# Kernel tuning notes

Measured on AMD Instinct MI355X. Metric: run time of the kernel, lower is better.

The kernel has to match this reference:

```python
import jax, jax.numpy as jnp
import numpy as np

D_MODEL = 1024
N_HEADS = 16
D_FF = 4096
EPS = 1e-5


def setup_inputs() -> dict:
    key = jax.random.key(0)
    ks = jax.random.split(key, 10)
    B, S, D, F = 4, 2048, D_MODEL, D_FF
    s = 0.02
    return {
        "x": jax.random.normal(ks[0], (B, S, D), jnp.float32),
        "Wq": jax.random.normal(ks[1], (D, D), jnp.float32) * s,
        "bq": jnp.zeros((D,), jnp.float32),
        "Wk": jax.random.normal(ks[2], (D, D), jnp.float32) * s,
        "bk": jnp.zeros((D,), jnp.float32),
        "Wv": jax.random.normal(ks[3], (D, D), jnp.float32) * s,
        "bv": jnp.zeros((D,), jnp.float32),
        "Wo": jax.random.normal(ks[4], (D, D), jnp.float32) * s,
        "bo": jnp.zeros((D,), jnp.float32),
        "ln1_g": jnp.ones((D,), jnp.float32),
        "ln1_b": jnp.zeros((D,), jnp.float32),
        "ln2_g": jnp.ones((D,), jnp.float32),
        "ln2_b": jnp.zeros((D,), jnp.float32),
        "W1": jax.random.normal(ks[5], (D, F), jnp.float32) * s,
        "b1": jnp.zeros((F,), jnp.float32),
        "W2": jax.random.normal(ks[6], (F, D), jnp.float32) * s,
        "b2": jnp.zeros((D,), jnp.float32),
    }


def _layernorm(x, g, b):
    mu = jnp.mean(x, axis=-1, keepdims=True)
    var = jnp.mean(jnp.square(x - mu), axis=-1, keepdims=True)
    return (x - mu) * jax.lax.rsqrt(var + EPS) * g + b


def _attention(x, Wq, bq, Wk, bk, Wv, bv, Wo, bo):
    B, S, D = x.shape
    H, dk = N_HEADS, D // N_HEADS
    q = (x @ Wq + bq).reshape(B, S, H, dk).transpose(0, 2, 1, 3)  # bhsd
    k = (x @ Wk + bk).reshape(B, S, H, dk).transpose(0, 2, 1, 3)
    v = (x @ Wv + bv).reshape(B, S, H, dk).transpose(0, 2, 1, 3)
    scale = 1.0 / np.sqrt(dk)
    scores = jnp.einsum("bhqd,bhkd->bhqk", q, k) * scale
    causal = jnp.tril(jnp.ones((S, S), bool))
    scores = jnp.where(causal, scores, -jnp.inf)
    attn = jax.nn.softmax(scores, axis=-1)
    out = jnp.einsum("bhqk,bhkd->bhqd", attn, v)
    out = out.transpose(0, 2, 1, 3).reshape(B, S, D)
    return out @ Wo + bo


def reference(x, Wq, bq, Wk, bk, Wv, bv, Wo, bo, ln1_g, ln1_b, ln2_g, ln2_b, W1, b1, W2, b2):
    # Pre-LN: x -> LN -> attn -> +x -> LN -> FFN -> +x  (dropout = eval/identity)
    attn_out = _attention(_layernorm(x, ln1_g, ln1_b), Wq, bq, Wk, bk, Wv, bv, Wo, bo)
    x = x + attn_out
    h = _layernorm(x, ln2_g, ln2_b)
    ffn = jax.nn.gelu(h @ W1 + b1, approximate=False) @ W2 + b2
    return x + ffn
```

## Files before the change

### kernel.cpp

```cpp
#include <hip/hip_runtime.h>
#include <hip/hip_bf16.h>
#include <math.h>

typedef __attribute__((ext_vector_type(8))) short short8;
typedef __attribute__((ext_vector_type(4))) float floatx4;
typedef __attribute__((ext_vector_type(4))) short short4v;
typedef __attribute__((ext_vector_type(2))) unsigned int uint2v;

#define D_MODEL 1024
#define N_HEADS 16
#define DK 64
#define D_FF 4096
#define BB 4
#define SS 2048
#define NTOK (BB * SS)
#define LN_EPS 1e-5f
#define SCL 0.18033688011112042f

static __device__ __forceinline__ short f2bf(float f) {
  union { float f; unsigned int u; } v;
  v.f = f;
  unsigned int u = v.u;
  unsigned int r = u + 0x7fffu + ((u >> 16) & 1u);
  return (short)(r >> 16);
}

#define GLL16(g, l)                                                            \
  __builtin_amdgcn_global_load_lds(                                            \
      (const __attribute__((address_space(1))) void*)(g),                      \
      (__attribute__((address_space(3))) void*)(l), 16, 0, 0)

__global__ __launch_bounds__(256) void ln_kernel(const float* __restrict__ x,
                                                 const float* __restrict__ g,
                                                 const float* __restrict__ b,
                                                 short* __restrict__ out) {
  int row = blockIdx.x;
  int t = threadIdx.x;
  const float4* rp = (const float4*)(x + (size_t)row * D_MODEL);
  float4 v = rp[t];
  float s = v.x + v.y + v.z + v.w;
  float ss = v.x * v.x + v.y * v.y + v.z * v.z + v.w * v.w;
#pragma unroll
  for (int off = 32; off >= 1; off >>= 1) {
    s += __shfl_xor(s, off, 64);
    ss += __shfl_xor(ss, off, 64);
  }
  __shared__ float red[8];
  int wv = t >> 6;
  if ((t & 63) == 0) { red[wv] = s; red[wv + 4] = ss; }
  __syncthreads();
  s = red[0] + red[1] + red[2] + red[3];
  ss = red[4] + red[5] + red[6] + red[7];
  float mu = s * (1.0f / D_MODEL);
  float var = ss * (1.0f / D_MODEL) - mu * mu;
  float rstd = rsqrtf(var + LN_EPS);
  float4 gv = ((const float4*)g)[t];
  float4 bv = ((const float4*)b)[t];
  short4v o;
  o.x = f2bf((v.x - mu) * rstd * gv.x + bv.x);
  o.y = f2bf((v.y - mu) * rstd * gv.y + bv.y);
  o.z = f2bf((v.z - mu) * rstd * gv.z + bv.z);
  o.w = f2bf((v.w - mu) * rstd * gv.w + bv.w);
  *(short4v*)(out + (size_t)row * D_MODEL + t * 4) = o;
}

__global__ __launch_bounds__(256) void wconvert_all(
    const float* __restrict__ Wq, const float* __restrict__ Wk,
    const float* __restrict__ Wv, const float* __restrict__ Wo,
    const float* __restrict__ W1, const float* __restrict__ W2,
    const float* __restrict__ bq, const float* __restrict__ bk,
    const float* __restrict__ bv,
    short* __restrict__ wqkv_t, short* __restrict__ wo_t,
    short* __restrict__ w1_t, short* __restrict__ w2_t,
    float* __restrict__ bqkv) {
  __shared__ float tile[64][65];
  int id = blockIdx.x;
  int t = threadIdx.x;
  if (id == 3072) {
    for (int i = t; i < 1024; i += 256) {
      bqkv[i] = bq[i] * SCL;
      bqkv[1024 + i] = bk[i];
      bqkv[2048 + i] = bv[i];
    }
    return;
  }
  const float* W;
  short* Wt;
  int K, N, tid;
  float scale = 1.0f;
  if (id < 1024) {
    int wsel = id >> 8;
    tid = id & 255;
    K = 1024; N = 1024;
    W = wsel == 0 ? Wq : wsel == 1 ? Wk : wsel == 2 ? Wv : Wo;
    Wt = wsel < 3 ? wqkv_t + (size_t)wsel * 1024 * 1024 : wo_t;
    if (wsel == 0) scale = SCL;
  } else if (id < 2048) {
    tid = id - 1024; K = 1024; N = 4096; W = W1; Wt = w1_t;
  } else {
    tid = id - 2048; K = 4096; N = 1024; W = W2; Wt = w2_t;
  }
  int ntn = N >> 6;
  int n0 = (tid % ntn) * 64, k0 = (tid / ntn) * 64;
  int c = t & 63, r0 = t >> 6;
#pragma unroll
  for (int i = 0; i < 16; i++) {
    int r = r0 + i * 4;
    tile[r][c] = W[(size_t)(k0 + r) * N + n0 + c];
  }
  __syncthreads();
#pragma unroll
  for (int i = 0; i < 16; i++) {
    int r = r0 + i * 4;
    Wt[(size_t)(n0 + r) * K + k0 + c] = f2bf(tile[c][r] * scale);
  }
}

template <int MODE>
__global__ __launch_bounds__(256, 4) void gemm_bt(const short* __restrict__ A,
                                                  const short* __restrict__ Bt,
                                                  const float* __restrict__ bias,
                                                  const float* __restrict__ res,
                                                  float* __restrict__ outf,
                                                  short* __restrict__ outb,
                                                  int M, int N, int K) {
  __shared__ short As[128 * 64];
  __shared__ short Bs[128 * 64];
  int t = threadIdx.x;
  int w = t >> 6, l = t & 63;
  int lm = l & 15, lq = l >> 4;
  int nx = gridDim.x;
  int id = blockIdx.y * nx + blockIdx.x;
  int xcd = id & 7;
  int k = id >> 3;
  int rows_per = gridDim.y >> 3;
  int mt = xcd * rows_per + k / nx;
  int nt = k - (k / nx) * nx;
  int m0 = mt * 128, n0 = nt * 128;
  floatx4 acc[4][4] = {};
  int l3 = l >> 3;
  int c7 = ((l & 7) ^ l3) * 8;
  const short* aA = A + (size_t)(m0 + w * 8 + l3) * K + c7;
  const short* aB = Bt + (size_t)(n0 + w * 8 + l3) * K + c7;
  int wm = (w & 1) * 64, wn = (w >> 1) * 64;
  int sw = lm & 7;

  for (int kt = 0; kt < K; kt += 64) {
#pragma unroll
    for (int j = 0; j < 4; j++) {
      GLL16(aA + (size_t)(j * 32) * K, As + (j * 32 + w * 8) * 64);
      GLL16(aB + (size_t)(j * 32) * K, Bs + (j * 32 + w * 8) * 64);
    }
    aA += 64;
    aB += 64;
    __syncthreads();
#pragma unroll
    for (int kk = 0; kk < 2; kk++) {
      int rdoff = ((kk * 4 + lq) ^ sw) * 8;
      short8 af[4], bfr[4];
#pragma unroll
      for (int mi = 0; mi < 4; mi++)
        af[mi] = *(const short8*)&As[(wm + mi * 16 + lm) * 64 + rdoff];
#pragma unroll
      for (int ni = 0; ni < 4; ni++)
        bfr[ni] = *(const short8*)&Bs[(wn + ni * 16 + lm) * 64 + rdoff];
#pragma unroll
      for (int mi = 0; mi < 4; mi++)
#pragma unroll
        for (int ni = 0; ni < 4; ni++)
          acc[mi][ni] = __builtin_amdgcn_mfma_f32_16x16x32_bf16(af[mi], bfr[ni],
                                                                acc[mi][ni], 0, 0, 0);
    }
    __syncthreads();
  }

#pragma unroll
  for (int mi = 0; mi < 4; mi++) {
#pragma unroll
    for (int ni = 0; ni < 4; ni++) {
      int col = n0 + wn + ni * 16 + lm;
      float bcol = bias[col];
#pragma unroll
      for (int r = 0; r < 4; r++) {
        int row = m0 + wm + mi * 16 + lq * 4 + r;
        float v = acc[mi][ni][r] + bcol;
        size_t idx = (size_t)row * N + col;
        if (MODE == 0) {
          outb[idx] = f2bf(v);
        } else if (MODE == 1) {
          outf[idx] = v + res[idx];
        } else {
          float vc = v + 0.044715f * v * v * v;
          float e = __builtin_amdgcn_exp2f(2.302265246314f * vc);
          float ge = v * e * __builtin_amdgcn_rcpf(e + 1.0f);
          outb[idx] = f2bf(ge);
        }
      }
    }
  }
}

__global__ __launch_bounds__(256) void vtrans(const short* __restrict__ qkv,
                                              short* __restrict__ vt) {
  __shared__ short Ls[64][72];
  int t = threadIdx.x;
  int s0 = blockIdx.x * 64;
  int bh = blockIdx.y;
  int b = bh >> 4, h = bh & 15;
  const short* vsrc = qkv + (size_t)b * SS * 3072 + 2048 + h * 64;
#pragma unroll
  for (int it = 0; it < 2; it++) {
    int idx = it * 256 + t;
    int sr = idx >> 3, ch = idx & 7;
    *(short8*)&Ls[sr][ch * 8] =
        *(const short8*)&vsrc[(size_t)(s0 + sr) * 3072 + ch * 8];
  }
  __syncthreads();
  int d = t >> 2, sb = (t & 3) * 16;
  short tmp[16];
#pragma unroll
  for (int j = 0; j < 16; j++) tmp[j] = Ls[sb + j][d];
  short8* dst = (short8*)&vt[(size_t)bh * DK * SS + (size_t)d * SS + s0 + sb];
  dst[0] = *(short8*)&tmp[0];
  dst[1] = *(short8*)&tmp[8];
}

__global__ __launch_bounds__(256, 3) void attn_kernel(const short* __restrict__ qkv,
                                                      const short* __restrict__ vt,
                                                      short* __restrict__ o) {
  __shared__ short Qs[128 * 64];
  __shared__ short Ks[64 * 64];
  __shared__ short Vs[80 * 64];
  __shared__ short Ps[128 * 72];
  int t = threadIdx.x, w = t >> 6, l = t & 63;
  int bh = blockIdx.x;
  int qi = 15 - blockIdx.y;
  int b = bh >> 4, h = bh & 15;
  const short* qbase = qkv + (size_t)b * SS * 3072 + h * DK;
  const short* kbase = qbase + 1024;
  const short* vbase = vt + (size_t)bh * DK * SS;
  short* obase = o + (size_t)b * SS * D_MODEL + h * DK;
  int l7 = l & 7, l3 = l >> 3;
  int c7 = (l7 ^ l3) * 8;
  int lm = l & 15, lq = l >> 4;
  int swq = lm & 7;
  int q0 = qi * 128;

  {
    int r = 64 + (t >> 4);
    int c = (t & 15) * 4;
    short val = (r == 64) ? (short)0x3F80 : (short)0;
    short4v vv = {val, val, val, val};
    *(short4v*)&Vs[r * 64 + c] = vv;
  }
#pragma unroll
  for (int j = 0; j < 4; j++) {
    int r8 = w * 32 + j * 8;
    GLL16(qbase + (size_t)(q0 + r8 + l3) * 3072 + c7, Qs + r8 * 64);
  }
  __syncthreads();
  short8 aq[2][2];
#pragma unroll
  for (int m = 0; m < 2; m++)
#pragma unroll
    for (int hf = 0; hf < 2; hf++)
      aq[m][hf] = *(const short8*)&Qs[(w * 32 + m * 16 + lm) * 64 +
                                      ((hf * 4 + lq) ^ swq) * 8];

  floatx4 accO[2][4] = {};
  floatx4 accL[2] = {};
  int qrow[2] = {q0 + w * 32 + lm, q0 + w * 32 + 16 + lm};
  int wrow_min = q0 + w * 32;
  int wrow_max = wrow_min + 31;
  int ntile = 2 * qi + 2;
  for (int kt = 0; kt < ntile; kt++) {
    int k0 = kt * 64;
    __syncthreads();
#pragma unroll
    for (int j = 0; j < 2; j++) {
      int r8 = (w * 2 + j) * 8;
      GLL16(kbase + (size_t)(k0 + r8 + l3) * 3072 + c7, Ks + r8 * 64);
      GLL16(vbase + (size_t)(r8 + l3) * SS + k0 + c7, Vs + r8 * 64);
    }
    __syncthreads();

    if (k0 <= wrow_max) {
      floatx4 sc[4][2];
#pragma unroll
      for (int sb = 0; sb < 4; sb++) {
        short8 k0f = *(const short8*)&Ks[(sb * 16 + lm) * 64 + (lq ^ swq) * 8];
        short8 k1f =
            *(const short8*)&Ks[(sb * 16 + lm) * 64 + ((4 + lq) ^ swq) * 8];
#pragma unroll
        for (int m = 0; m < 2; m++) {
          floatx4 z = {};
          z = __builtin_amdgcn_mfma_f32_16x16x32_bf16(k0f, aq[m][0], z, 0, 0, 0);
          z = __builtin_amdgcn_mfma_f32_16x16x32_bf16(k1f, aq[m][1], z, 0, 0, 0);
          sc[sb][m] = z;
        }
      }
      if (k0 + 63 <= wrow_min) {
#pragma unroll
        for (int sb = 0; sb < 4; sb++)
#pragma unroll
          for (int m = 0; m < 2; m++)
#pragma unroll
            for (int r = 0; r < 4; r++)
              sc[sb][m][r] = __builtin_amdgcn_exp2f(sc[sb][m][r]);
      } else {
#pragma unroll
        for (int sb = 0; sb < 4; sb++) {
          int sbase = k0 + sb * 16 + lq * 4;
#pragma unroll
          for (int m = 0; m < 2; m++)
#pragma unroll
            for (int r = 0; r < 4; r++)
              sc[sb][m][r] = (sbase + r > qrow[m])
                                 ? 0.f
                                 : __builtin_amdgcn_exp2f(sc[sb][m][r]);
        }
      }
#pragma unroll
      for (int m = 0; m < 2; m++)
#pragma unroll
        for (int sb = 0; sb < 4; sb++) {
          union { float f; unsigned int u; } c0, c1, c2, c3;
          c0.f = sc[sb][m][0]; c1.f = sc[sb][m][1];
          c2.f = sc[sb][m][2]; c3.f = sc[sb][m][3];
          uint2v pk;
          pk.x = __builtin_amdgcn_perm(c1.u, c0.u, 0x07060302u);
          pk.y = __builtin_amdgcn_perm(c3.u, c2.u, 0x07060302u);
          *(uint2v*)&Ps[(w * 32 + m * 16 + lm) * 72 + sb * 16 + lq * 4] = pk;
        }
      short8 pa[2][2];
#pragma unroll
      for (int m = 0; m < 2; m++)
#pragma unroll
        for (int hf = 0; hf < 2; hf++)
          pa[m][hf] =
              *(const short8*)&Ps[(w * 32 + m * 16 + lm) * 72 + hf * 32 + lq * 8];
      short8 o0 = *(const short8*)&Vs[(64 + lm) * 64 + (lq ^ swq) * 8];
      short8 o1 = *(const short8*)&Vs[(64 + lm) * 64 + ((4 + lq) ^ swq) * 8];
#pragma unroll
      for (int m = 0; m < 2; m++) {
        accL[m] = __builtin_amdgcn_mfma_f32_16x16x32_bf16(pa[m][0], o0, accL[m], 0, 0, 0);
        accL[m] = __builtin_amdgcn_mfma_f32_16x16x32_bf16(pa[m][1], o1, accL[m], 0, 0, 0);
      }
#pragma unroll
      for (int nb = 0; nb < 4; nb++) {
        short8 v0f = *(const short8*)&Vs[(nb * 16 + lm) * 64 + (lq ^ swq) * 8];
        short8 v1f =
            *(const short8*)&Vs[(nb * 16 + lm) * 64 + ((4 + lq) ^ swq) * 8];
#pragma unroll
        for (int m = 0; m < 2; m++) {
          accO[m][nb] = __builtin_amdgcn_mfma_f32_16x16x32_bf16(pa[m][0], v0f,
                                                                accO[m][nb], 0, 0, 0);
          accO[m][nb] = __builtin_amdgcn_mfma_f32_16x16x32_bf16(pa[m][1], v1f,
                                                                accO[m][nb], 0, 0, 0);
        }
      }
    }
  }
#pragma unroll
  for (int m = 0; m < 2; m++) {
#pragma unroll
    for (int r = 0; r < 4; r++) {
      float lv = __shfl(accL[m][r], l & 48, 64);
      float invr = __builtin_amdgcn_rcpf(lv);
      int rowg = q0 + w * 32 + m * 16 + lq * 4 + r;
#pragma unroll
      for (int nb = 0; nb < 4; nb++)
        obase[(size_t)rowg * D_MODEL + nb * 16 + lm] = f2bf(accO[m][nb][r] * invr);
    }
  }
}

extern "C" void kernel_launch(void* const* d_in, const int* in_sizes, int n_in,
                              void* d_out, int out_size, void* d_ws, size_t ws_size,
                              hipStream_t stream) {
  const float* x = (const float*)d_in[0];
  const float* Wq = (const float*)d_in[1];
  const float* bq = (const float*)d_in[2];
  const float* Wk = (const float*)d_in[3];
  const float* bk = (const float*)d_in[4];
  const float* Wv = (const float*)d_in[5];
  const float* bv = (const float*)d_in[6];
  const float* Wo = (const float*)d_in[7];
  const float* bo = (const float*)d_in[8];
  const float* ln1g = (const float*)d_in[9];
  const float* ln1b = (const float*)d_in[10];
  const float* ln2g = (const float*)d_in[11];
  const float* ln2b = (const float*)d_in[12];
  const float* W1 = (const float*)d_in[13];
  const float* b1 = (const float*)d_in[14];
  const float* W2 = (const float*)d_in[15];
  const float* b2 = (const float*)d_in[16];
  float* out = (float*)d_out;

  short* wqkv_t = (short*)d_ws;
  short* wo_t = wqkv_t + 3072 * 1024;
  short* w1_t = wo_t + 1024 * 1024;
  short* w2_t = w1_t + 4096 * 1024;
  float* bqkv = (float*)(w2_t + 1024 * 4096);
  short* h_bf = (short*)(bqkv + 3072);
  short* qkvb = h_bf + (size_t)NTOK * D_MODEL;
  short* vtg = qkvb + (size_t)NTOK * 3072;
  short* ffn1 = qkvb;

  wconvert_all<<<3073, 256, 0, stream>>>(Wq, Wk, Wv, Wo, W1, W2, bq, bk, bv,
                                         wqkv_t, wo_t, w1_t, w2_t, bqkv);

  ln_kernel<<<NTOK, 256, 0, stream>>>(x, ln1g, ln1b, h_bf);

  gemm_bt<0><<<dim3(24, 64), 256, 0, stream>>>(h_bf, wqkv_t, bqkv, nullptr, nullptr,
                                               qkvb, NTOK, 3072, 1024);

  vtrans<<<dim3(SS / 64, 64), 256, 0, stream>>>(qkvb, vtg);

  attn_kernel<<<dim3(64, 16), 256, 0, stream>>>(qkvb, vtg, h_bf);

  gemm_bt<1><<<dim3(8, 64), 256, 0, stream>>>(h_bf, wo_t, bo, x, out, nullptr,
                                              NTOK, 1024, 1024);

  ln_kernel<<<NTOK, 256, 0, stream>>>(out, ln2g, ln2b, h_bf);

  gemm_bt<2><<<dim3(32, 64), 256, 0, stream>>>(h_bf, w1_t, b1, nullptr, nullptr,
                                               ffn1, NTOK, 4096, 1024);

  gemm_bt<1><<<dim3(8, 64), 256, 0, stream>>>(ffn1, w2_t, b2, out, out, nullptr,
                                              NTOK, 1024, 4096);
}
```

Measured before the change: 465.8 us.

## Fuse all stages into one persistent cooperative kernel with grid syncs

```diff
diff --git a/kernel.cpp b/kernel.cpp
--- a/kernel.cpp
+++ b/kernel.cpp
@@ -1,6 +1,9 @@
 #include <hip/hip_runtime.h>
 #include <hip/hip_bf16.h>
+#include <hip/hip_cooperative_groups.h>
 #include <math.h>
+
+namespace cg = cooperative_groups;
 
 typedef __attribute__((ext_vector_type(8))) short short8;
 typedef __attribute__((ext_vector_type(4))) float floatx4;
@@ -16,6 +19,7 @@
 #define NTOK (BB * SS)
 #define LN_EPS 1e-5f
 #define SCL 0.18033688011112042f
+#define NBLK 768
 
 static __device__ __forceinline__ short f2bf(float f) {
   union { float f; unsigned int u; } v;
@@ -30,11 +34,11 @@
       (const __attribute__((address_space(1))) void*)(g),                      \
       (__attribute__((address_space(3))) void*)(l), 16, 0, 0)
 
-__global__ __launch_bounds__(256) void ln_kernel(const float* __restrict__ x,
-                                                 const float* __restrict__ g,
-                                                 const float* __restrict__ b,
-                                                 short* __restrict__ out) {
-  int row = blockIdx.x;
+
+__device__ __forceinline__ void dev_ln_row(int row, const float* x,
+                                           const float* g, const float* b,
+                                           short* out, char* smem) {
+  float* red = (float*)smem;
   int t = threadIdx.x;
   const float4* rp = (const float4*)(x + (size_t)row * D_MODEL);
   float4 v = rp[t];
@@ -45,7 +49,6 @@
     s += __shfl_xor(s, off, 64);
     ss += __shfl_xor(ss, off, 64);
   }
-  __shared__ float red[8];
   int wv = t >> 6;
   if ((t & 63) == 0) { red[wv] = s; red[wv + 4] = ss; }
   __syncthreads();
@@ -64,17 +67,11 @@
   *(short4v*)(out + (size_t)row * D_MODEL + t * 4) = o;
 }
 
-__global__ __launch_bounds__(256) void wconvert_all(
-    const float* __restrict__ Wq, const float* __restrict__ Wk,
-    const float* __restrict__ Wv, const float* __restrict__ Wo,
-    const float* __restrict__ W1, const float* __restrict__ W2,
-    const float* __restrict__ bq, const float* __restrict__ bk,
-    const float* __restrict__ bv,
-    short* __restrict__ wqkv_t, short* __restrict__ wo_t,
-    short* __restrict__ w1_t, short* __restrict__ w2_t,
-    float* __restrict__ bqkv) {
-  __shared__ float tile[64][65];
-  int id = blockIdx.x;
+__device__ __forceinline__ void dev_wconv(
+    int id, const float* Wq, const float* Wk, const float* Wv, const float* Wo,
+    const float* W1, const float* W2, const float* bq, const float* bk,
+    const float* bv, short* wqkv_t, short* wo_t, short* w1_t, short* w2_t,
+    float* bqkv, char* smem) {
   int t = threadIdx.x;
   if (id == 3072) {
     for (int i = t; i < 1024; i += 256) {
@@ -84,6 +81,7 @@
     }
     return;
   }
+  float (*tile)[65] = (float (*)[65])smem;
   const float* W;
   short* Wt;
   int K, N, tid;
@@ -117,26 +115,14 @@
 }
 
 template <int MODE>
-__global__ __launch_bounds__(256, 4) void gemm_bt(const short* __restrict__ A,
-                                                  const short* __restrict__ Bt,
-                                                  const float* __restrict__ bias,
-                                                  const float* __restrict__ res,
-                                                  float* __restrict__ outf,
-                                                  short* __restrict__ outb,
-                                                  int M, int N, int K) {
-  __shared__ short As[128 * 64];
-  __shared__ short Bs[128 * 64];
+__device__ __forceinline__ void dev_gemm_tile(
+    const short* A, const short* Bt, const float* bias, const float* res,
+    float* outf, short* outb, int N, int K, int m0, int n0, char* smem) {
+  short* As = (short*)smem;
+  short* Bs = As + 128 * 64;
   int t = threadIdx.x;
   int w = t >> 6, l = t & 63;
   int lm = l & 15, lq = l >> 4;
-  int nx = gridDim.x;
-  int id = blockIdx.y * nx + blockIdx.x;
-  int xcd = id & 7;
-  int k = id >> 3;
-  int rows_per = gridDim.y >> 3;
-  int mt = xcd * rows_per + k / nx;
-  int nt = k - (k / nx) * nx;
-  int m0 = mt * 128, n0 = nt * 128;
   floatx4 acc[4][4] = {};
   int l3 = l >> 3;
   int c7 = ((l & 7) ^ l3) * 8;
@@ -200,12 +186,27 @@
   }
 }
 
-__global__ __launch_bounds__(256) void vtrans(const short* __restrict__ qkv,
-                                              short* __restrict__ vt) {
-  __shared__ short Ls[64][72];
+template <int MODE>
+__device__ __forceinline__ void dev_gemm_stage(
+    const short* A, const short* Bt, const float* bias, const float* res,
+    float* outf, short* outb, int M, int N, int K, char* smem, int b0) {
+  int nx = N >> 7, ny = M >> 7;
+  int per_xcd = (nx * ny) >> 3;
+  int rows_per = ny >> 3;
+  int xcd = b0 & 7, slot = b0 >> 3;
+  for (int k2 = slot; k2 < per_xcd; k2 += 96) {
+    int mt = xcd * rows_per + k2 / nx;
+    int nt = k2 % nx;
+    dev_gemm_tile<MODE>(A, Bt, bias, res, outf, outb, N, K, mt << 7, nt << 7, smem);
+  }
+}
+
+__device__ __forceinline__ void dev_vtrans(int item, const short* qkv,
+                                           short* vt, char* smem) {
+  short (*Ls)[72] = (short (*)[72])smem;
   int t = threadIdx.x;
-  int s0 = blockIdx.x * 64;
-  int bh = blockIdx.y;
+  int s0 = (item & 31) * 64;
+  int bh = item >> 5;
   int b = bh >> 4, h = bh & 15;
   const short* vsrc = qkv + (size_t)b * SS * 3072 + 2048 + h * 64;
 #pragma unroll
@@ -223,18 +224,18 @@
   short8* dst = (short8*)&vt[(size_t)bh * DK * SS + (size_t)d * SS + s0 + sb];
   dst[0] = *(short8*)&tmp[0];
   dst[1] = *(short8*)&tmp[8];
-}
-
-__global__ __launch_bounds__(256, 3) void attn_kernel(const short* __restrict__ qkv,
-                                                      const short* __restrict__ vt,
-                                                      short* __restrict__ o) {
-  __shared__ short Qs[128 * 64];
-  __shared__ short Ks[64 * 64];
-  __shared__ short Vs[80 * 64];
-  __shared__ short Ps[128 * 72];
+  __syncthreads();
+}
+
+__device__ __forceinline__ void dev_attn(int item, const short* qkv,
+                                         const short* vt, short* o, char* smem) {
+  short* Qs = (short*)smem;
+  short* Ks = Qs + 128 * 64;
+  short* Vs = Ks + 64 * 64;
+  short* Ps = Vs + 80 * 64;
   int t = threadIdx.x, w = t >> 6, l = t & 63;
-  int bh = blockIdx.x;
-  int qi = 15 - blockIdx.y;
+  int bh = item & 63;
+  int qi = 15 - (item >> 6);
   int b = bh >> 4, h = bh & 15;
   const short* qbase = qkv + (size_t)b * SS * 3072 + h * DK;
   const short* kbase = qbase + 1024;
@@ -246,6 +247,7 @@
   int swq = lm & 7;
   int q0 = qi * 128;
 
+  __syncthreads();
   {
     int r = 64 + (t >> 4);
     int c = (t & 15) * 4;
@@ -373,6 +375,96 @@
         obase[(size_t)rowg * D_MODEL + nb * 16 + lm] = f2bf(accO[m][nb][r] * invr);
     }
   }
+}
+
+struct MegaArgs {
+  const float *x, *Wq, *bq, *Wk, *bk, *Wv, *bv, *Wo, *bo;
+  const float *ln1g, *ln1b, *ln2g, *ln2b, *W1, *b1, *W2, *b2;
+  float* out;
+  short *wqkv_t, *wo_t, *w1_t, *w2_t;
+  float* bqkv;
+  short *h_bf, *qkvb, *vtg, *ffn1;
+};
+
+__global__ __launch_bounds__(256, 3) void mega_kernel(MegaArgs a) {
+  __shared__ __align__(16) char smem[53248];
+  cg::grid_group grid = cg::this_grid();
+  int b0 = blockIdx.x;
+
+  for (int id = b0; id < 3073 + NTOK; id += NBLK) {
+    if (id < 3073)
+      dev_wconv(id, a.Wq, a.Wk, a.Wv, a.Wo, a.W1, a.W2, a.bq, a.bk, a.bv,
+                a.wqkv_t, a.wo_t, a.w1_t, a.w2_t, a.bqkv, smem);
+    else
+      dev_ln_row(id - 3073, a.x, a.ln1g, a.ln1b, a.h_bf, smem);
+    __syncthreads();
+  }
+  grid.sync();
+  dev_gemm_stage<0>(a.h_bf, a.wqkv_t, a.bqkv, nullptr, nullptr, a.qkvb,
+                    NTOK, 3072, 1024, smem, b0);
+  grid.sync();
+  for (int id = b0; id < 2048; id += NBLK)
+    dev_vtrans(id, a.qkvb, a.vtg, smem);
+  grid.sync();
+  dev_attn(b0, a.qkvb, a.vtg, a.h_bf, smem);
+  if (b0 >= 512) dev_attn(1535 - b0, a.qkvb, a.vtg, a.h_bf, smem);
+  grid.sync();
+  dev_gemm_stage<1>(a.h_bf, a.wo_t, a.bo, a.x, a.out, nullptr,
+                    NTOK, 1024, 1024, smem, b0);
+  grid.sync();
+  for (int id = b0; id < NTOK; id += NBLK) {
+    dev_ln_row(id, a.out, a.ln2g, a.ln2b, a.h_bf, smem);
+    __syncthreads();
+  }
+  grid.sync();
+  dev_gemm_stage<2>(a.h_bf, a.w1_t, a.b1, nullptr, nullptr, a.ffn1,
+                    NTOK, 4096, 1024, smem, b0);
+  grid.sync();
+  dev_gemm_stage<1>(a.ffn1, a.w2_t, a.b2, a.out, a.out, nullptr,
+                    NTOK, 1024, 4096, smem, b0);
+}
+
+__global__ __launch_bounds__(256) void ln_kernel(const float* x, const float* g,
+                                                 const float* b, short* out) {
+  __shared__ __align__(16) char smem[64];
+  dev_ln_row(blockIdx.x, x, g, b, out, smem);
+}
+
+__global__ __launch_bounds__(256) void wconvert_all(
+    const float* Wq, const float* Wk, const float* Wv, const float* Wo,
+    const float* W1, const float* W2, const float* bq, const float* bk,
+    const float* bv, short* wqkv_t, short* wo_t, short* w1_t, short* w2_t,
+    float* bqkv) {
+  __shared__ __align__(16) char smem[64 * 65 * 4];
+  dev_wconv(blockIdx.x, Wq, Wk, Wv, Wo, W1, W2, bq, bk, bv, wqkv_t, wo_t, w1_t,
+            w2_t, bqkv, smem);
+}
+
+template <int MODE>
+__global__ __launch_bounds__(256, 4) void gemm_bt(const short* A, const short* Bt,
+                                                  const float* bias,
+                                                  const float* res, float* outf,
+                                                  short* outb, int M, int N, int K) {
+  __shared__ __align__(16) char smem[32768];
+  int nx = gridDim.x;
+  int id = blockIdx.y * nx + blockIdx.x;
+  int xcd = id & 7;
+  int k = id >> 3;
+  int rows_per = gridDim.y >> 3;
+  int mt = xcd * rows_per + k / nx;
+  int nt = k - (k / nx) * nx;
+  dev_gemm_tile<MODE>(A, Bt, bias, res, outf, outb, N, K, mt * 128, nt * 128, smem);
+}
+
+__global__ __launch_bounds__(256) void vtrans(const short* qkv, short* vt) {
+  __shared__ __align__(16) char smem[64 * 72 * 2];
+  dev_vtrans(blockIdx.y * 32 + blockIdx.x, qkv, vt, smem);
+}
+
+__global__ __launch_bounds__(256, 3) void attn_kernel(const short* qkv,
+                                                      const short* vt, short* o) {
+  __shared__ __align__(16) char smem[53248];
+  dev_attn(blockIdx.y * 64 + blockIdx.x, qkv, vt, o, smem);
 }
 
 extern "C" void kernel_launch(void* const* d_in, const int* in_sizes, int n_in,
@@ -407,26 +499,29 @@
   short* vtg = qkvb + (size_t)NTOK * 3072;
   short* ffn1 = qkvb;
 
+  MegaArgs a;
+  a.x = x; a.Wq = Wq; a.bq = bq; a.Wk = Wk; a.bk = bk; a.Wv = Wv; a.bv = bv;
+  a.Wo = Wo; a.bo = bo; a.ln1g = ln1g; a.ln1b = ln1b; a.ln2g = ln2g;
+  a.ln2b = ln2b; a.W1 = W1; a.b1 = b1; a.W2 = W2; a.b2 = b2; a.out = out;
+  a.wqkv_t = wqkv_t; a.wo_t = wo_t; a.w1_t = w1_t; a.w2_t = w2_t;
+  a.bqkv = bqkv; a.h_bf = h_bf; a.qkvb = qkvb; a.vtg = vtg; a.ffn1 = ffn1;
+  void* kp[1] = {&a};
+  hipError_t err = hipLaunchCooperativeKernel((void*)mega_kernel, dim3(NBLK),
+                                              dim3(256), kp, 0, stream);
+  if (err == hipSuccess) return;
+
   wconvert_all<<<3073, 256, 0, stream>>>(Wq, Wk, Wv, Wo, W1, W2, bq, bk, bv,
                                          wqkv_t, wo_t, w1_t, w2_t, bqkv);
-
   ln_kernel<<<NTOK, 256, 0, stream>>>(x, ln1g, ln1b, h_bf);
-
-  gemm_bt<0><<<dim3(24, 64), 256, 0, stream>>>(h_bf, wqkv_t, bqkv, nullptr, nullptr,
-                                               qkvb, NTOK, 3072, 1024);
-
-  vtrans<<<dim3(SS / 64, 64), 256, 0, stream>>>(qkvb, vtg);
-
+  gemm_bt<0><<<dim3(24, 64), 256, 0, stream>>>(h_bf, wqkv_t, bqkv, nullptr,
+                                               nullptr, qkvb, NTOK, 3072, 1024);
+  vtrans<<<dim3(32, 64), 256, 0, stream>>>(qkvb, vtg);
   attn_kernel<<<dim3(64, 16), 256, 0, stream>>>(qkvb, vtg, h_bf);
-
   gemm_bt<1><<<dim3(8, 64), 256, 0, stream>>>(h_bf, wo_t, bo, x, out, nullptr,
                                               NTOK, 1024, 1024);
-
   ln_kernel<<<NTOK, 256, 0, stream>>>(out, ln2g, ln2b, h_bf);
-
   gemm_bt<2><<<dim3(32, 64), 256, 0, stream>>>(h_bf, w1_t, b1, nullptr, nullptr,
                                                ffn1, NTOK, 4096, 1024);
-
   gemm_bt<1><<<dim3(8, 64), 256, 0, stream>>>(ffn1, w2_t, b2, out, out, nullptr,
                                               NTOK, 1024, 4096);
 }
```

Result: slower. 1.134 ms (+143.5%).

## Split-K the FFN down-projection with atomic adds and fuse LN1 into weight prep

Applied to the files above, without the earlier changes.

```diff
diff --git a/kernel.cpp b/kernel.cpp
--- a/kernel.cpp
+++ b/kernel.cpp
@@ -30,11 +30,10 @@
       (const __attribute__((address_space(1))) void*)(g),                      \
       (__attribute__((address_space(3))) void*)(l), 16, 0, 0)
 
-__global__ __launch_bounds__(256) void ln_kernel(const float* __restrict__ x,
-                                                 const float* __restrict__ g,
-                                                 const float* __restrict__ b,
-                                                 short* __restrict__ out) {
-  int row = blockIdx.x;
+__device__ __forceinline__ void ln_row(int row, const float* __restrict__ x,
+                                       const float* __restrict__ g,
+                                       const float* __restrict__ b,
+                                       short* __restrict__ out, float* red) {
   int t = threadIdx.x;
   const float4* rp = (const float4*)(x + (size_t)row * D_MODEL);
   float4 v = rp[t];
@@ -45,7 +44,6 @@
     s += __shfl_xor(s, off, 64);
     ss += __shfl_xor(ss, off, 64);
   }
-  __shared__ float red[8];
   int wv = t >> 6;
   if ((t & 63) == 0) { red[wv] = s; red[wv + 4] = ss; }
   __syncthreads();
@@ -64,18 +62,31 @@
   *(short4v*)(out + (size_t)row * D_MODEL + t * 4) = o;
 }
 
-__global__ __launch_bounds__(256) void wconvert_all(
+__global__ __launch_bounds__(256) void ln_kernel(const float* __restrict__ x,
+                                                 const float* __restrict__ g,
+                                                 const float* __restrict__ b,
+                                                 short* __restrict__ out) {
+  __shared__ float red[8];
+  ln_row(blockIdx.x, x, g, b, out, red);
+}
+
+__global__ __launch_bounds__(256) void prep_kernel(
     const float* __restrict__ Wq, const float* __restrict__ Wk,
     const float* __restrict__ Wv, const float* __restrict__ Wo,
     const float* __restrict__ W1, const float* __restrict__ W2,
     const float* __restrict__ bq, const float* __restrict__ bk,
-    const float* __restrict__ bv,
+    const float* __restrict__ bv, const float* __restrict__ x,
+    const float* __restrict__ ln1g, const float* __restrict__ ln1b,
     short* __restrict__ wqkv_t, short* __restrict__ wo_t,
     short* __restrict__ w1_t, short* __restrict__ w2_t,
-    float* __restrict__ bqkv) {
-  __shared__ float tile[64][65];
+    float* __restrict__ bqkv, short* __restrict__ h_bf) {
+  __shared__ __align__(16) float smem[64 * 65];
   int id = blockIdx.x;
   int t = threadIdx.x;
+  if (id >= 3073) {
+    ln_row(id - 3073, x, ln1g, ln1b, h_bf, smem);
+    return;
+  }
   if (id == 3072) {
     for (int i = t; i < 1024; i += 256) {
       bqkv[i] = bq[i] * SCL;
@@ -84,6 +95,7 @@
     }
     return;
   }
+  float (*tile)[65] = (float (*)[65])smem;
   const float* W;
   short* Wt;
   int K, N, tid;
@@ -123,7 +135,8 @@
                                                   const float* __restrict__ res,
                                                   float* __restrict__ outf,
                                                   short* __restrict__ outb,
-                                                  int M, int N, int K) {
+                                                  int M, int N, int Kloop,
+                                                  int ldK) {
   __shared__ short As[128 * 64];
   __shared__ short Bs[128 * 64];
   int t = threadIdx.x;
@@ -137,19 +150,22 @@
   int mt = xcd * rows_per + k / nx;
   int nt = k - (k / nx) * nx;
   int m0 = mt * 128, n0 = nt * 128;
+  int kz = blockIdx.z;
+  const short* Az = A + (size_t)kz * Kloop;
+  const short* Btz = Bt + (size_t)kz * Kloop;
   floatx4 acc[4][4] = {};
   int l3 = l >> 3;
   int c7 = ((l & 7) ^ l3) * 8;
-  const short* aA = A + (size_t)(m0 + w * 8 + l3) * K + c7;
-  const short* aB = Bt + (size_t)(n0 + w * 8 + l3) * K + c7;
+  const short* aA = Az + (size_t)(m0 + w * 8 + l3) * ldK + c7;
+  const short* aB = Btz + (size_t)(n0 + w * 8 + l3) * ldK + c7;
   int wm = (w & 1) * 64, wn = (w >> 1) * 64;
   int sw = lm & 7;
 
-  for (int kt = 0; kt < K; kt += 64) {
+  for (int kt = 0; kt < Kloop; kt += 64) {
 #pragma unroll
     for (int j = 0; j < 4; j++) {
-      GLL16(aA + (size_t)(j * 32) * K, As + (j * 32 + w * 8) * 64);
-      GLL16(aB + (size_t)(j * 32) * K, Bs + (j * 32 + w * 8) * 64);
+      GLL16(aA + (size_t)(j * 32) * ldK, As + (j * 32 + w * 8) * 64);
+      GLL16(aB + (size_t)(j * 32) * ldK, Bs + (j * 32 + w * 8) * 64);
     }
     aA += 64;
     aB += 64;
@@ -174,12 +190,13 @@
     __syncthreads();
   }
 
+  bool addb = (MODE != 3) || (kz == 0);
 #pragma unroll
   for (int mi = 0; mi < 4; mi++) {
 #pragma unroll
     for (int ni = 0; ni < 4; ni++) {
       int col = n0 + wn + ni * 16 + lm;
-      float bcol = bias[col];
+      float bcol = addb ? bias[col] : 0.0f;
 #pragma unroll
       for (int r = 0; r < 4; r++) {
         int row = m0 + wm + mi * 16 + lq * 4 + r;
@@ -189,11 +206,13 @@
           outb[idx] = f2bf(v);
         } else if (MODE == 1) {
           outf[idx] = v + res[idx];
-        } else {
+        } else if (MODE == 2) {
           float vc = v + 0.044715f * v * v * v;
           float e = __builtin_amdgcn_exp2f(2.302265246314f * vc);
           float ge = v * e * __builtin_amdgcn_rcpf(e + 1.0f);
           outb[idx] = f2bf(ge);
+        } else {
+          atomicAdd(&outf[idx], v);
         }
       }
     }
@@ -407,26 +426,19 @@
   short* vtg = qkvb + (size_t)NTOK * 3072;
   short* ffn1 = qkvb;
 
-  wconvert_all<<<3073, 256, 0, stream>>>(Wq, Wk, Wv, Wo, W1, W2, bq, bk, bv,
-                                         wqkv_t, wo_t, w1_t, w2_t, bqkv);
-
-  ln_kernel<<<NTOK, 256, 0, stream>>>(x, ln1g, ln1b, h_bf);
-
-  gemm_bt<0><<<dim3(24, 64), 256, 0, stream>>>(h_bf, wqkv_t, bqkv, nullptr, nullptr,
-                                               qkvb, NTOK, 3072, 1024);
-
+  prep_kernel<<<3073 + NTOK, 256, 0, stream>>>(Wq, Wk, Wv, Wo, W1, W2, bq, bk,
+                                               bv, x, ln1g, ln1b, wqkv_t, wo_t,
+                                               w1_t, w2_t, bqkv, h_bf);
+  gemm_bt<0><<<dim3(24, 64), 256, 0, stream>>>(h_bf, wqkv_t, bqkv, nullptr,
+                                               nullptr, qkvb, NTOK, 3072, 1024,
+                                               1024);
   vtrans<<<dim3(SS / 64, 64), 256, 0, stream>>>(qkvb, vtg);
-
   attn_kernel<<<dim3(64, 16), 256, 0, stream>>>(qkvb, vtg, h_bf);
-
   gemm_bt<1><<<dim3(8, 64), 256, 0, stream>>>(h_bf, wo_t, bo, x, out, nullptr,
-                                              NTOK, 1024, 1024);
-
+                                              NTOK, 1024, 1024, 1024);
   ln_kernel<<<NTOK, 256, 0, stream>>>(out, ln2g, ln2b, h_bf);
-
   gemm_bt<2><<<dim3(32, 64), 256, 0, stream>>>(h_bf, w1_t, b1, nullptr, nullptr,
-                                               ffn1, NTOK, 4096, 1024);
-
-  gemm_bt<1><<<dim3(8, 64), 256, 0, stream>>>(ffn1, w2_t, b2, out, out, nullptr,
-                                              NTOK, 1024, 4096);
-}
+                                               ffn1, NTOK, 4096, 1024, 1024);
+  gemm_bt<3><<<dim3(8, 64, 2), 256, 0, stream>>>(ffn1, w2_t, b2, nullptr, out,
+                                                 nullptr, NTOK, 1024, 2048, 4096);
+}
```

Measured after the change: 451.6 us. 3.0% less time.
